# Kernel optimization log

Measured on AMD Instinct MI355X. Metric: run time of the kernel, lower is better.

## Reference

```python
import jax, jax.numpy as jnp
import numpy as np

S, B, D, E, F = 2048, 2, 1024, 8, 4096


def setup_inputs() -> dict:
    key = jax.random.key(0)
    ks = jax.random.split(key, 6)
    x = jax.random.normal(ks[0], (S, B, D), dtype=jnp.float32)
    w_switch = jax.random.normal(ks[1], (D, E), dtype=jnp.float32) / np.sqrt(D)
    b_switch = jnp.zeros((E,), dtype=jnp.float32)
    w1 = jax.random.normal(ks[2], (E, D, F), dtype=jnp.float32) / np.sqrt(D)
    b1 = jnp.zeros((E, F), dtype=jnp.float32)
    w2 = jax.random.normal(ks[3], (E, F, D), dtype=jnp.float32) / np.sqrt(F)
    b2 = jnp.zeros((E, D), dtype=jnp.float32)
    return {"x": x, "w_switch": w_switch, "b_switch": b_switch,
            "w1": w1, "b1": b1, "w2": w2, "b2": b2}


def reference(x, w_switch, b_switch, w1, b1, w2, b2):
    # x: [S, B, D] -> tokens [N, D]
    s, b, d = x.shape
    n_experts = w1.shape[0]
    xf = x.reshape(-1, d)                                    # [N, D]
    route_prob = jax.nn.softmax(xf @ w_switch + b_switch, axis=-1)  # [N, E]
    route_prob_max = jnp.max(route_prob, axis=-1)            # [N]
    routes = jnp.argmax(route_prob, axis=-1)                 # [N] int
    # is_scale_prob=True: scale token by its routing probability before FFN
    xs = xf * route_prob_max[:, None]                        # [N, D]
    # Per-expert FFN evaluated densely (drop_tokens=False => every token kept),
    # then each token selects its routed expert's output.
    h = jax.nn.relu(jnp.einsum('nd,edf->enf', xs, w1) + b1[:, None, :])  # [E, N, F]
    y = jnp.einsum('enf,efd->end', h, w2) + b2[:, None, :]               # [E, N, D]
    n = xf.shape[0]
    out = y[routes, jnp.arange(n)]                           # [N, D]
    counts = jnp.zeros((n_experts,), dtype=jnp.float32).at[routes].add(1.0)
    n_dropped = jnp.zeros((), dtype=jnp.int32)               # drop_tokens=False
    return out.reshape(s, b, d), counts, route_prob.sum(0), n_dropped
```

## Files before the change

### kernel.cpp

```cpp
#include <hip/hip_runtime.h>
#include <hip/hip_bf16.h>

#define NTOK 4096
#define DDIM 1024
#define NEXP 8
#define FDIM 4096
#define MAXTILES 40

typedef __attribute__((ext_vector_type(4))) float f32x4;
typedef __attribute__((ext_vector_type(8))) short bf16x8;

#define GLDS(g, l) __builtin_amdgcn_global_load_lds( \
    (const __attribute__((address_space(1))) unsigned int*)(g), \
    (__attribute__((address_space(3))) unsigned int*)(l), 16, 0, 0)

__global__ __launch_bounds__(256) void route_kernel(
    const float* __restrict__ x,
    const float* __restrict__ w_switch,
    const float* __restrict__ b_switch,
    __hip_bfloat16* __restrict__ xs,
    int* __restrict__ amax_arr,
    float* __restrict__ partial)
{
    const int tid = threadIdx.x;
    const int wave = tid >> 6, lane = tid & 63;
    __shared__ float pr[4][16];

    float wacc[16];
#pragma unroll
    for (int j = 0; j < 16; j++) wacc[j] = 0.0f;

    for (int i = 0; i < 4; i++) {
        const int n = blockIdx.x * 16 + wave * 4 + i;
        const float4* xr = (const float4*)(x + (size_t)n * DDIM);
        float4 xv[4];
#pragma unroll
        for (int j = 0; j < 4; j++) xv[j] = xr[lane + j * 64];

        float acc[NEXP];
#pragma unroll
        for (int e = 0; e < NEXP; e++) acc[e] = 0.0f;
#pragma unroll
        for (int j = 0; j < 4; j++) {
            const int dbase = (lane + j * 64) * 4;
#pragma unroll
            for (int c = 0; c < 4; c++) {
                const float4* wr = (const float4*)(w_switch + (size_t)(dbase + c) * NEXP);
                float4 w0 = wr[0], w1 = wr[1];
                float xvc = ((const float*)&xv[j])[c];
                acc[0] += xvc * w0.x; acc[1] += xvc * w0.y;
                acc[2] += xvc * w0.z; acc[3] += xvc * w0.w;
                acc[4] += xvc * w1.x; acc[5] += xvc * w1.y;
                acc[6] += xvc * w1.z; acc[7] += xvc * w1.w;
            }
        }
#pragma unroll
        for (int e = 0; e < NEXP; e++) {
            float v = acc[e];
#pragma unroll
            for (int off = 32; off > 0; off >>= 1) v += __shfl_xor(v, off, 64);
            acc[e] = v;
        }
        float mx = -1e30f;
#pragma unroll
        for (int e = 0; e < NEXP; e++) {
            acc[e] += b_switch[e];
            mx = fmaxf(mx, acc[e]);
        }
        float sum = 0.0f;
#pragma unroll
        for (int e = 0; e < NEXP; e++) { acc[e] = __expf(acc[e] - mx); sum += acc[e]; }
        float inv = 1.0f / sum;
        float pmax = -1.0f; int amax = 0;
#pragma unroll
        for (int e = 0; e < NEXP; e++) {
            float p = acc[e] * inv;
            acc[e] = p;
            if (p > pmax) { pmax = p; amax = e; }
        }
#pragma unroll
        for (int e = 0; e < NEXP; e++) {
            wacc[e] += acc[e];
            wacc[8 + e] += (amax == e) ? 1.0f : 0.0f;
        }
        if (lane == 0) amax_arr[n] = amax;
#pragma unroll
        for (int j = 0; j < 4; j++) {
            ushort4 pk;
            __hip_bfloat16* pp = (__hip_bfloat16*)&pk;
            pp[0] = __float2bfloat16(xv[j].x * pmax);
            pp[1] = __float2bfloat16(xv[j].y * pmax);
            pp[2] = __float2bfloat16(xv[j].z * pmax);
            pp[3] = __float2bfloat16(xv[j].w * pmax);
            *(ushort4*)(xs + (size_t)n * DDIM + (lane + j * 64) * 4) = pk;
        }
    }
    if (lane == 0) {
#pragma unroll
        for (int j = 0; j < 16; j++) pr[wave][j] = wacc[j];
    }
    __syncthreads();
    if (tid < 16)
        partial[blockIdx.x * 16 + tid] = pr[0][tid] + pr[1][tid] + pr[2][tid] + pr[3][tid];
}

__global__ __launch_bounds__(1024) void bucket_finalize_kernel(
    const int* __restrict__ amax_arr, const float* __restrict__ partial,
    int* __restrict__ bucket, int* __restrict__ ecnt,
    float* __restrict__ out_tail, int* __restrict__ table)
{
    __shared__ int ctr[NEXP];
    __shared__ float red[16][16];
    if (threadIdx.x < NEXP) ctr[threadIdx.x] = 0;
    __syncthreads();
    const int lane = threadIdx.x & 63;
    for (int c = 0; c < NTOK; c += 1024) {
        int t = c + threadIdx.x;
        int a = amax_arr[t];
#pragma unroll
        for (int e = 0; e < NEXP; e++) {
            bool my = (a == e);
            unsigned long long mask = __ballot(my);
            int cnt = __popcll(mask);
            int base = 0;
            if (lane == 0 && cnt) base = atomicAdd(&ctr[e], cnt);
            base = __shfl(base, 0, 64);
            if (my) {
                int rank = __popcll(mask & ((1ull << lane) - 1ull));
                bucket[e * NTOK + base + rank] = t;
            }
        }
    }
    if (threadIdx.x < 256) {
        const int j = threadIdx.x & 15, g = threadIdx.x >> 4;
        float s = 0.0f;
        for (int k = 0; k < 16; k++) s += partial[(size_t)(g + k * 16) * 16 + j];
        red[g][j] = s;
    }
    __syncthreads();
    if (threadIdx.x < NEXP) ecnt[threadIdx.x] = ctr[threadIdx.x];
    if (threadIdx.x < 16) {
        float t2 = 0.0f;
        for (int k = 0; k < 16; k++) t2 += red[k][threadIdx.x];
        int dst = (threadIdx.x < 8) ? (8 + threadIdx.x) : (threadIdx.x - 8);
        out_tail[dst] = t2;
    }
    if (threadIdx.x == 16) out_tail[16] = 0.0f;
    if (threadIdx.x == 0) {
        int idx = 0;
        for (int e = 0; e < NEXP; e++) {
            int cnt2 = ctr[e];
            for (int m0 = 0; m0 < cnt2; m0 += 128) table[idx++] = (e << 16) | m0;
        }
        for (; idx < MAXTILES; idx++) table[idx] = -1;
    }
}

template <int R, int C>
__global__ __launch_bounds__(256) void transpose_kernel(
    const float* __restrict__ in, __hip_bfloat16* __restrict__ outp)
{
    const int e = blockIdx.z;
    const int r0 = blockIdx.y * 128, c0 = blockIdx.x * 128;
    __shared__ __align__(16) __hip_bfloat16 t[128 * 128];
    const int tid = threadIdx.x;

    const float* src = in + ((size_t)e * R + r0) * C + c0;
#pragma unroll
    for (int k = 0; k < 16; k++) {
        const int id = k * 256 + tid;
        const int row = id >> 5, colq = id & 31;
        float4 v = *(const float4*)(src + (size_t)row * C + colq * 4);
        ushort4 pk;
        __hip_bfloat16* pp = (__hip_bfloat16*)&pk;
        pp[0] = __float2bfloat16(v.x); pp[1] = __float2bfloat16(v.y);
        pp[2] = __float2bfloat16(v.z); pp[3] = __float2bfloat16(v.w);
        const int b = (row * 256 + colq * 8) ^ (((row >> 3) & 1) << 6);
        *(ushort4*)((char*)t + b) = pk;
    }
    __syncthreads();

    const int rb = tid & 15, cb = tid >> 4;
    unsigned v[8][4];
#pragma unroll
    for (int i = 0; i < 8; i++) {
        const int row = rb * 8 + i;
        const int b = (row * 256 + cb * 16) ^ ((rb & 1) << 6);
        *(uint4*)v[i] = *(const uint4*)((const char*)t + b);
    }
    __hip_bfloat16* dst = outp + ((size_t)e * C + c0 + cb * 8) * R + r0 + rb * 8;
#pragma unroll
    for (int j = 0; j < 8; j++) {
        const unsigned sel = (j & 1) ? 0x07060302u : 0x05040100u;
        unsigned o[4];
#pragma unroll
        for (int w = 0; w < 4; w++)
            o[w] = __builtin_amdgcn_perm(v[2 * w + 1][j >> 1], v[2 * w][j >> 1], sel);
        *(uint4*)(dst + (size_t)j * R) = *(uint4*)o;
    }
}

template <int MODE, int K, int NN, int KS, int NX>
__device__ __forceinline__ void gemm_body(
    const __hip_bfloat16* __restrict__ A,
    const __hip_bfloat16* __restrict__ Bt,
    const float* __restrict__ bias,
    const int* __restrict__ bucket,
    const int* __restrict__ ecnt,
    const int* __restrict__ table,
    void* __restrict__ Out)
{
    const int bid = blockIdx.x;
    const int xcd = bid & 7;
    const int q = bid >> 3;
    const int x = q % NX;
    const int yk = (q / NX) % (MAXTILES / 8);
    const int z = q / (NX * (MAXTILES / 8));
    const int y = xcd + 8 * yk;

    const int entry = table[y];
    if (entry < 0) return;
    const int e = entry >> 16;
    const int m0 = entry & 0xffff;
    const int cnt = ecnt[e];
    const int n0 = x * 128;
    const int kbase = (K / KS) * z;

    __shared__ __align__(16) __hip_bfloat16 Asm[128 * 64];
    __shared__ __align__(16) __hip_bfloat16 Bsm[128 * 64];
    __shared__ int toks[128];

    const int tid = threadIdx.x;
    if (tid < 128) {
        int r = m0 + tid;
        toks[tid] = bucket[e * NTOK + (r < cnt ? r : cnt - 1)];
    }
    __syncthreads();

    const int wave = tid >> 6, lane = tid & 63;
    const int srow = lane >> 3;
    const int swzcol = ((lane & 7) ^ srow) * 16;

    const char* pA[4];
#pragma unroll
    for (int i = 0; i < 4; i++)
        pA[i] = (const char*)(A + (size_t)toks[wave * 32 + i * 8 + srow] * K + kbase) + swzcol;
    const char* pB = (const char*)(Bt + ((size_t)e * NN + n0 + wave * 32 + srow) * K + kbase) + swzcol;

    const int wm = wave & 1, wn = wave >> 1;
    const int r16 = lane & 15, kq16 = lane >> 4;
    const int r7x = (r16 & 7) * 16;

    f32x4 acc[4][4];
#pragma unroll
    for (int t = 0; t < 4; t++)
#pragma unroll
        for (int u = 0; u < 4; u++) acc[t][u] = (f32x4){0.f, 0.f, 0.f, 0.f};

    for (int k0 = 0; k0 < K / KS; k0 += 64) {
#pragma unroll
        for (int i = 0; i < 4; i++) {
            GLDS(pA[i], (char*)Asm + (wave * 32 + i * 8) * 128 + lane * 16);
            GLDS(pB + (size_t)i * 8 * K * 2, (char*)Bsm + (wave * 32 + i * 8) * 128 + lane * 16);
            pA[i] += 128;
        }
        pB += 128;
        __syncthreads();

#pragma unroll
        for (int ksub = 0; ksub < 2; ksub++) {
            const int slot = ((kq16 + ksub * 4) * 16) ^ r7x;
            bf16x8 a[4], b[4];
#pragma unroll
            for (int t = 0; t < 4; t++)
                a[t] = *(const bf16x8*)((const char*)Asm +
                        (wm * 64 + t * 16 + r16) * 128 + slot);
#pragma unroll
            for (int u = 0; u < 4; u++)
                b[u] = *(const bf16x8*)((const char*)Bsm +
                        (wn * 64 + u * 16 + r16) * 128 + slot);
#pragma unroll
            for (int t = 0; t < 4; t++)
#pragma unroll
                for (int u = 0; u < 4; u++)
                    acc[t][u] = __builtin_amdgcn_mfma_f32_16x16x32_bf16(a[t], b[u], acc[t][u], 0, 0, 0);
        }
        __syncthreads();
    }

    const int quad = lane >> 4, l15 = lane & 15;
    float bv[4];
#pragma unroll
    for (int u = 0; u < 4; u++) {
        if (MODE == 0)
            bv[u] = bias[(size_t)e * NN + n0 + wn * 64 + u * 16 + l15];
        else
            bv[u] = (z == 0) ? bias[(size_t)e * NN + n0 + wn * 64 + u * 16 + l15] : 0.0f;
    }
#pragma unroll
    for (int t = 0; t < 4; t++) {
#pragma unroll
        for (int rr = 0; rr < 4; rr++) {
            int row = wm * 64 + t * 16 + quad * 4 + rr;
            if (m0 + row < cnt) {
                int tok = toks[row];
#pragma unroll
                for (int u = 0; u < 4; u++) {
                    int col = n0 + wn * 64 + u * 16 + l15;
                    float v = acc[t][u][rr] + bv[u];
                    if (MODE == 0) {
                        v = fmaxf(v, 0.0f);
                        ((__hip_bfloat16*)Out)[(size_t)tok * NN + col] = __float2bfloat16(v);
                    } else {
                        unsafeAtomicAdd(&((float*)Out)[(size_t)tok * NN + col], v);
                    }
                }
            }
        }
    }
}

__global__ __launch_bounds__(256, 4) void gemm_ffn1(
    const __hip_bfloat16* __restrict__ A, const __hip_bfloat16* __restrict__ Bt,
    const float* __restrict__ bias, const int* __restrict__ bucket,
    const int* __restrict__ ecnt, const int* __restrict__ table, void* __restrict__ Out)
{
    gemm_body<0, DDIM, FDIM, 1, FDIM / 128>(A, Bt, bias, bucket, ecnt, table, Out);
}

__global__ __launch_bounds__(256, 4) void gemm_ffn2(
    const __hip_bfloat16* __restrict__ A, const __hip_bfloat16* __restrict__ Bt,
    const float* __restrict__ bias, const int* __restrict__ bucket,
    const int* __restrict__ ecnt, const int* __restrict__ table, void* __restrict__ Out)
{
    gemm_body<1, FDIM, DDIM, 4, DDIM / 128>(A, Bt, bias, bucket, ecnt, table, Out);
}

extern "C" void kernel_launch(void* const* d_in, const int* in_sizes, int n_in,
                              void* d_out, int out_size, void* d_ws, size_t ws_size,
                              hipStream_t stream) {
    const float* x        = (const float*)d_in[0];
    const float* w_switch = (const float*)d_in[1];
    const float* b_switch = (const float*)d_in[2];
    const float* w1       = (const float*)d_in[3];
    const float* b1       = (const float*)d_in[4];
    const float* w2       = (const float*)d_in[5];
    const float* b2       = (const float*)d_in[6];

    float* out = (float*)d_out;
    float* out_tail = out + (size_t)NTOK * DDIM;

    char* ws = (char*)d_ws;
    __hip_bfloat16* xs = (__hip_bfloat16*)(ws);
    __hip_bfloat16* h  = (__hip_bfloat16*)(ws + 8388608ull);
    __hip_bfloat16* wt = (__hip_bfloat16*)(ws + 41943040ull);
    int* bucket        = (int*)(ws + 109051904ull);
    int* amax_arr      = (int*)(ws + 109182976ull);
    float* partial     = (float*)(ws + 109199360ull);
    int* ecnt          = (int*)(ws + 109215744ull);
    int* table         = (int*)(ws + 109215776ull);

    hipMemsetAsync(out, 0, (size_t)NTOK * DDIM * sizeof(float), stream);

    hipLaunchKernelGGL(route_kernel, dim3(256), dim3(256), 0, stream,
                       x, w_switch, b_switch, xs, amax_arr, partial);
    hipLaunchKernelGGL(bucket_finalize_kernel, dim3(1), dim3(1024), 0, stream,
                       amax_arr, partial, bucket, ecnt, out_tail, table);

    hipLaunchKernelGGL((transpose_kernel<DDIM, FDIM>), dim3(FDIM / 128, DDIM / 128, NEXP),
                       dim3(256), 0, stream, w1, wt);
    hipLaunchKernelGGL(gemm_ffn1, dim3((FDIM / 128) * MAXTILES), dim3(256), 0, stream,
                       xs, wt, b1, bucket, ecnt, table, (void*)h);

    hipLaunchKernelGGL((transpose_kernel<FDIM, DDIM>), dim3(DDIM / 128, FDIM / 128, NEXP),
                       dim3(256), 0, stream, w2, wt);
    hipLaunchKernelGGL(gemm_ffn2, dim3((DDIM / 128) * MAXTILES * 4), dim3(256), 0, stream,
                       h, wt, b2, bucket, ecnt, table, (void*)out);
}
```

Measured before the change: 480.8 us.

## Fuse weight fp32-to-bf16 conversion and transpose into GEMM B-tile loading

Removes the two separate transpose/convert kernels that wrote bf16 transposed copies of w1 and w2 to workspace. The GEMMs now read fp32 weights directly with register loads, convert them to bf16 and write them transposed into swizzled LDS. This drops a full read/write pass over the 64M-element weights and two launches. The cost is that each weight tile is re-read in fp32 (double the bytes) by every M-tile that uses it, and B loads go through registers instead of async global-to-LDS.

New measurement: 518.3 us. 1.08x slower.

```diff
diff --git a/kernel.cpp b/kernel.cpp
--- a/kernel.cpp
+++ b/kernel.cpp
@@ -156,54 +156,10 @@
     }
 }
 
-template <int R, int C>
-__global__ __launch_bounds__(256) void transpose_kernel(
-    const float* __restrict__ in, __hip_bfloat16* __restrict__ outp)
-{
-    const int e = blockIdx.z;
-    const int r0 = blockIdx.y * 128, c0 = blockIdx.x * 128;
-    __shared__ __align__(16) __hip_bfloat16 t[128 * 128];
-    const int tid = threadIdx.x;
-
-    const float* src = in + ((size_t)e * R + r0) * C + c0;
-#pragma unroll
-    for (int k = 0; k < 16; k++) {
-        const int id = k * 256 + tid;
-        const int row = id >> 5, colq = id & 31;
-        float4 v = *(const float4*)(src + (size_t)row * C + colq * 4);
-        ushort4 pk;
-        __hip_bfloat16* pp = (__hip_bfloat16*)&pk;
-        pp[0] = __float2bfloat16(v.x); pp[1] = __float2bfloat16(v.y);
-        pp[2] = __float2bfloat16(v.z); pp[3] = __float2bfloat16(v.w);
-        const int b = (row * 256 + colq * 8) ^ (((row >> 3) & 1) << 6);
-        *(ushort4*)((char*)t + b) = pk;
-    }
-    __syncthreads();
-
-    const int rb = tid & 15, cb = tid >> 4;
-    unsigned v[8][4];
-#pragma unroll
-    for (int i = 0; i < 8; i++) {
-        const int row = rb * 8 + i;
-        const int b = (row * 256 + cb * 16) ^ ((rb & 1) << 6);
-        *(uint4*)v[i] = *(const uint4*)((const char*)t + b);
-    }
-    __hip_bfloat16* dst = outp + ((size_t)e * C + c0 + cb * 8) * R + r0 + rb * 8;
-#pragma unroll
-    for (int j = 0; j < 8; j++) {
-        const unsigned sel = (j & 1) ? 0x07060302u : 0x05040100u;
-        unsigned o[4];
-#pragma unroll
-        for (int w = 0; w < 4; w++)
-            o[w] = __builtin_amdgcn_perm(v[2 * w + 1][j >> 1], v[2 * w][j >> 1], sel);
-        *(uint4*)(dst + (size_t)j * R) = *(uint4*)o;
-    }
-}
-
 template <int MODE, int K, int NN, int KS, int NX>
 __device__ __forceinline__ void gemm_body(
     const __hip_bfloat16* __restrict__ A,
-    const __hip_bfloat16* __restrict__ Bt,
+    const float* __restrict__ W,
     const float* __restrict__ bias,
     const int* __restrict__ bucket,
     const int* __restrict__ ecnt,
@@ -238,14 +194,23 @@
     __syncthreads();
 
     const int wave = tid >> 6, lane = tid & 63;
+
     const int srow = lane >> 3;
     const int swzcol = ((lane & 7) ^ srow) * 16;
-
     const char* pA[4];
 #pragma unroll
     for (int i = 0; i < 4; i++)
         pA[i] = (const char*)(A + (size_t)toks[wave * 32 + i * 8 + srow] * K + kbase) + swzcol;
-    const char* pB = (const char*)(Bt + ((size_t)e * NN + n0 + wave * 32 + srow) * K + kbase) + swzcol;
+
+    const int ng = tid & 31;
+    const int kg = tid >> 5;
+    const float* pW = W + ((size_t)e * K + kbase + kg * 8) * NN + n0 + ng * 4;
+    unsigned bofs[4];
+#pragma unroll
+    for (int c = 0; c < 4; c++) {
+        const int n = ng * 4 + c;
+        bofs[c] = n * 128 + ((kg ^ (n & 7)) * 16);
+    }
 
     const int wm = wave & 1, wn = wave >> 1;
     const int r16 = lane & 15, kq16 = lane >> 4;
@@ -261,10 +226,20 @@
 #pragma unroll
         for (int i = 0; i < 4; i++) {
             GLDS(pA[i], (char*)Asm + (wave * 32 + i * 8) * 128 + lane * 16);
-            GLDS(pB + (size_t)i * 8 * K * 2, (char*)Bsm + (wave * 32 + i * 8) * 128 + lane * 16);
             pA[i] += 128;
         }
-        pB += 128;
+        float4 v[8];
+#pragma unroll
+        for (int j = 0; j < 8; j++) v[j] = *(const float4*)(pW + (size_t)j * NN);
+        pW += (size_t)64 * NN;
+#pragma unroll
+        for (int c = 0; c < 4; c++) {
+            __hip_bfloat16 row[8];
+#pragma unroll
+            for (int j = 0; j < 8; j++)
+                row[j] = __float2bfloat16(((const float*)&v[j])[c]);
+            *(uint4*)((char*)Bsm + bofs[c]) = *(const uint4*)row;
+        }
         __syncthreads();
 
 #pragma unroll
@@ -307,12 +282,12 @@
 #pragma unroll
                 for (int u = 0; u < 4; u++) {
                     int col = n0 + wn * 64 + u * 16 + l15;
-                    float v = acc[t][u][rr] + bv[u];
+                    float vv = acc[t][u][rr] + bv[u];
                     if (MODE == 0) {
-                        v = fmaxf(v, 0.0f);
-                        ((__hip_bfloat16*)Out)[(size_t)tok * NN + col] = __float2bfloat16(v);
+                        vv = fmaxf(vv, 0.0f);
+                        ((__hip_bfloat16*)Out)[(size_t)tok * NN + col] = __float2bfloat16(vv);
                     } else {
-                        unsafeAtomicAdd(&((float*)Out)[(size_t)tok * NN + col], v);
+                        unsafeAtomicAdd(&((float*)Out)[(size_t)tok * NN + col], vv);
                     }
                 }
             }
@@ -321,19 +296,19 @@
 }
 
 __global__ __launch_bounds__(256, 4) void gemm_ffn1(
-    const __hip_bfloat16* __restrict__ A, const __hip_bfloat16* __restrict__ Bt,
+    const __hip_bfloat16* __restrict__ A, const float* __restrict__ W,
     const float* __restrict__ bias, const int* __restrict__ bucket,
     const int* __restrict__ ecnt, const int* __restrict__ table, void* __restrict__ Out)
 {
-    gemm_body<0, DDIM, FDIM, 1, FDIM / 128>(A, Bt, bias, bucket, ecnt, table, Out);
+    gemm_body<0, DDIM, FDIM, 1, FDIM / 128>(A, W, bias, bucket, ecnt, table, Out);
 }
 
 __global__ __launch_bounds__(256, 4) void gemm_ffn2(
-    const __hip_bfloat16* __restrict__ A, const __hip_bfloat16* __restrict__ Bt,
+    const __hip_bfloat16* __restrict__ A, const float* __restrict__ W,
     const float* __restrict__ bias, const int* __restrict__ bucket,
     const int* __restrict__ ecnt, const int* __restrict__ table, void* __restrict__ Out)
 {
-    gemm_body<1, FDIM, DDIM, 4, DDIM / 128>(A, Bt, bias, bucket, ecnt, table, Out);
+    gemm_body<1, FDIM, DDIM, 4, DDIM / 128>(A, W, bias, bucket, ecnt, table, Out);
 }
 
 extern "C" void kernel_launch(void* const* d_in, const int* in_sizes, int n_in,
@@ -353,7 +328,6 @@
     char* ws = (char*)d_ws;
     __hip_bfloat16* xs = (__hip_bfloat16*)(ws);
     __hip_bfloat16* h  = (__hip_bfloat16*)(ws + 8388608ull);
-    __hip_bfloat16* wt = (__hip_bfloat16*)(ws + 41943040ull);
     int* bucket        = (int*)(ws + 109051904ull);
     int* amax_arr      = (int*)(ws + 109182976ull);
     float* partial     = (float*)(ws + 109199360ull);
@@ -367,13 +341,9 @@
     hipLaunchKernelGGL(bucket_finalize_kernel, dim3(1), dim3(1024), 0, stream,
                        amax_arr, partial, bucket, ecnt, out_tail, table);
 
-    hipLaunchKernelGGL((transpose_kernel<DDIM, FDIM>), dim3(FDIM / 128, DDIM / 128, NEXP),
-                       dim3(256), 0, stream, w1, wt);
     hipLaunchKernelGGL(gemm_ffn1, dim3((FDIM / 128) * MAXTILES), dim3(256), 0, stream,
-                       xs, wt, b1, bucket, ecnt, table, (void*)h);
-
-    hipLaunchKernelGGL((transpose_kernel<FDIM, DDIM>), dim3(DDIM / 128, FDIM / 128, NEXP),
-                       dim3(256), 0, stream, w2, wt);
+                       xs, w1, b1, bucket, ecnt, table, (void*)h);
+
     hipLaunchKernelGGL(gemm_ffn2, dim3((DDIM / 128) * MAXTILES * 4), dim3(256), 0, stream,
-                       h, wt, b2, bucket, ecnt, table, (void*)out);
-}
+                       h, w2, b2, bucket, ecnt, table, (void*)out);
+}
```
